# Performance work log

Measured on AMD Instinct MI355X. Metric: run time of the kernel, lower is better.

## Reference

```python
import jax, jax.numpy as jnp
import numpy as np

N = 100000
E = 1_600_000
IN_X, OUT_X = 128, 128
IN_E, OUT_E = 32, 128


def setup_inputs() -> dict:
    key = jax.random.key(0)
    k1, k2, k3, k4, k5, k6, k7 = jax.random.split(key, 7)
    x = jax.random.normal(k1, (N, IN_X), dtype=jnp.float32)
    edge_index = jax.random.randint(k2, (2, E), 0, N, dtype=jnp.int64)
    edge_attr = jax.random.normal(k3, (E, IN_E), dtype=jnp.float32)
    Wx = jax.random.normal(k4, (IN_X, OUT_X), dtype=jnp.float32) * (1.0 / np.sqrt(IN_X))
    bx = jax.random.normal(k5, (OUT_X,), dtype=jnp.float32) * 0.01
    We = jax.random.normal(k6, (IN_E, OUT_E), dtype=jnp.float32) * (1.0 / np.sqrt(IN_E))
    be = jax.random.normal(k7, (OUT_E,), dtype=jnp.float32) * 0.01
    return {"x": x, "edge_index": edge_index, "edge_attr": edge_attr,
            "Wx": Wx, "bx": bx, "We": We, "be": be}


def reference(x, edge_index, edge_attr, Wx, bx, We, be):
    # torch: to_dense() -> [N, N, in_e]; sum over dim=1 == scatter-add of
    # edge_attr into rows indexed by the source node edge_index[0].
    agg = jax.ops.segment_sum(edge_attr, edge_index[0], num_segments=x.shape[0])  # [N, in_e]
    hx = x @ Wx + bx          # [N, out_x]
    he = agg @ We + be        # [N, out_e]
    return jnp.concatenate((hx, he), axis=1)  # [N, out_x + out_e]
```

## Files before the change

kernel.cpp:

```cpp
#include <hip/hip_runtime.h>


#define BSHIFT    7
#define BSIZE     128
#define NBMAX     1024
#define SEG_CAP   3584
#define POOL_SZ   3648
#define CHUNK_A   8192
#define SPILL_CAP 65536

typedef short bf16x8 __attribute__((ext_vector_type(8)));
typedef float f32x4  __attribute__((ext_vector_type(4)));

__device__ __forceinline__ unsigned short f2bf(float f) {
    union { float f; unsigned u; } c; c.f = f;
    unsigned u = c.u;
    u += 0x7FFF + ((u >> 16) & 1);
    return (unsigned short)(u >> 16);
}

__global__ __launch_bounds__(512) void binA_kernel(
    const int* __restrict__ src, int E, int nb,
    unsigned* __restrict__ segs, int* __restrict__ gcnt,
    int2* __restrict__ spill, int* __restrict__ spillcnt)
{
    __shared__ unsigned pool[CHUNK_A];
    __shared__ int hist[NBMAX];
    __shared__ int offs[NBMAX];
    __shared__ int lcur[NBMAX];
    __shared__ int gbase[NBMAX];
    __shared__ int gallow[NBMAX];
    __shared__ int wsum[8];

    int tid = threadIdx.x;
    int base = blockIdx.x * CHUNK_A;

    for (int i = tid; i < NBMAX; i += 512) hist[i] = 0;
    __syncthreads();

    for (int i = tid; i < CHUNK_A; i += 512) {
        int e = base + i;
        if (e < E) atomicAdd(&hist[src[e] >> BSHIFT], 1);
    }
    __syncthreads();

    {
        int t2 = tid * 2;
        int c0 = hist[t2], c1 = hist[t2 + 1];
        int s = c0 + c1;
        int lane = tid & 63, wid = tid >> 6;
        int ws = s;
        #pragma unroll
        for (int d = 1; d < 64; d <<= 1) {
            int t = __shfl_up(ws, d);
            if (lane >= d) ws += t;
        }
        if (lane == 63) wsum[wid] = ws;
        __syncthreads();
        int woff = 0;
        #pragma unroll
        for (int w = 0; w < 8; ++w) if (w < wid) woff += wsum[w];
        int ex = woff + ws - s;
        offs[t2] = ex;          lcur[t2] = ex;
        offs[t2 + 1] = ex + c0; lcur[t2 + 1] = ex + c0;
    }
    __syncthreads();

    {
        int t2 = tid * 2;
        #pragma unroll
        for (int u = 0; u < 2; ++u) {
            int b = t2 + u;
            if (b < nb) {
                int cnt = hist[b];
                int b0 = cnt ? atomicAdd(&gcnt[b], cnt) : 0;
                gbase[b] = b0;
                int allow = SEG_CAP - b0;
                if (allow < 0) allow = 0;
                if (allow > cnt) allow = cnt;
                gallow[b] = allow;
            }
        }
    }
    __syncthreads();

    for (int i = tid; i < CHUNK_A; i += 512) {
        int e = base + i;
        if (e < E) {
            int s = src[e];
            int b = s >> BSHIFT;
            int p = atomicAdd(&lcur[b], 1);
            pool[p] = ((unsigned)e << BSHIFT) | (unsigned)(s & (BSIZE - 1));
        }
    }
    __syncthreads();

    int wid = tid >> 6, lane = tid & 63;
    for (int b = wid; b < nb; b += 8) {
        int cnt = hist[b];
        int off = offs[b];
        int allow = gallow[b];
        unsigned* dst = segs + (size_t)b * SEG_CAP + gbase[b];
        for (int i = lane; i < allow; i += 64)
            dst[i] = pool[off + i];
        int excess = cnt - allow;
        if (excess > 0) {
            int sb;
            if (lane == 0) sb = atomicAdd(spillcnt, excess);
            sb = __shfl(sb, 0);
            for (int i = lane; i < excess; i += 64) {
                int sp = sb + i;
                if (sp < SPILL_CAP) {
                    unsigned pv = pool[off + allow + i];
                    spill[sp] = make_int2((int)(pv >> BSHIFT),
                                          (b << BSHIFT) | (int)(pv & (BSIZE - 1)));
                }
            }
        }
    }
}

__global__ __launch_bounds__(512) void gather_kernel(
    const unsigned* __restrict__ segs, const int* __restrict__ gcnt,
    const int2* __restrict__ spill, const int* __restrict__ spillcnt,
    const float4* __restrict__ ea4, unsigned short* __restrict__ aggbf, int N)
{
    __shared__ int counts[BSIZE];
    __shared__ int starts[BSIZE + 1];
    __shared__ int cursor[BSIZE];
    __shared__ int pool[POOL_SZ];

    int tid = threadIdx.x;
    int b = blockIdx.x;
    int node0 = b << BSHIFT;

    if (tid < BSIZE) counts[tid] = 0;
    __syncthreads();

    int segn = gcnt[b]; if (segn > SEG_CAP) segn = SEG_CAP;
    const unsigned* seg = segs + (size_t)b * SEG_CAP;
    int nsp = *spillcnt; if (nsp > SPILL_CAP) nsp = SPILL_CAP;

    for (int i = tid; i < segn; i += 512)
        atomicAdd(&counts[seg[i] & (BSIZE - 1)], 1);
    if (nsp)
        for (int i = tid; i < nsp; i += 512) {
            int2 p = spill[i];
            if ((p.y >> BSHIFT) == b) atomicAdd(&counts[p.y & (BSIZE - 1)], 1);
        }
    __syncthreads();

    if (tid < 64) {
        int c0 = counts[tid * 2], c1 = counts[tid * 2 + 1];
        int s = c0 + c1;
        int ws = s;
        #pragma unroll
        for (int d = 1; d < 64; d <<= 1) {
            int t = __shfl_up(ws, d);
            if (tid >= d) ws += t;
        }
        int ex = ws - s;
        starts[tid * 2] = ex;          cursor[tid * 2] = ex;
        starts[tid * 2 + 1] = ex + c0; cursor[tid * 2 + 1] = ex + c0;
        if (tid == 63) starts[BSIZE] = ws;
    }
    __syncthreads();

    for (int i = tid; i < segn; i += 512) {
        unsigned pe = seg[i];
        int pos = atomicAdd(&cursor[pe & (BSIZE - 1)], 1);
        if (pos < POOL_SZ) pool[pos] = (int)(pe >> BSHIFT);
    }
    if (nsp)
        for (int i = tid; i < nsp; i += 512) {
            int2 p = spill[i];
            if ((p.y >> BSHIFT) == b) {
                int pos = atomicAdd(&cursor[p.y & (BSIZE - 1)], 1);
                if (pos < POOL_SZ) pool[pos] = p.x;
            }
        }
    __syncthreads();

    int g = tid >> 2, q2 = tid & 3;
    int node = node0 + g;
    if (node < N) {
        int p0 = starts[g], p1 = starts[g + 1];
        if (p1 > POOL_SZ) p1 = POOL_SZ;
        float4 aL0 = {0.f,0.f,0.f,0.f}, aL1 = {0.f,0.f,0.f,0.f};
        float4 aH0 = {0.f,0.f,0.f,0.f}, aH1 = {0.f,0.f,0.f,0.f};
        int p = p0;
        for (; p + 4 <= p1; p += 4) {
            int e0 = pool[p], e1 = pool[p + 1], e2 = pool[p + 2], e3 = pool[p + 3];
            const float4* r0 = ea4 + (size_t)e0 * 8;
            const float4* r1 = ea4 + (size_t)e1 * 8;
            const float4* r2 = ea4 + (size_t)e2 * 8;
            const float4* r3 = ea4 + (size_t)e3 * 8;
            float4 l0 = r0[q2],     l1 = r1[q2],     l2 = r2[q2],     l3 = r3[q2];
            float4 h0 = r0[q2 + 4], h1 = r1[q2 + 4], h2 = r2[q2 + 4], h3 = r3[q2 + 4];
            aL0.x += l0.x; aL0.y += l0.y; aL0.z += l0.z; aL0.w += l0.w;
            aL1.x += l1.x; aL1.y += l1.y; aL1.z += l1.z; aL1.w += l1.w;
            aH0.x += h0.x; aH0.y += h0.y; aH0.z += h0.z; aH0.w += h0.w;
            aH1.x += h1.x; aH1.y += h1.y; aH1.z += h1.z; aH1.w += h1.w;
            aL0.x += l2.x; aL0.y += l2.y; aL0.z += l2.z; aL0.w += l2.w;
            aL1.x += l3.x; aL1.y += l3.y; aL1.z += l3.z; aL1.w += l3.w;
            aH0.x += h2.x; aH0.y += h2.y; aH0.z += h2.z; aH0.w += h2.w;
            aH1.x += h3.x; aH1.y += h3.y; aH1.z += h3.z; aH1.w += h3.w;
        }
        for (; p < p1; ++p) {
            const float4* r = ea4 + (size_t)pool[p] * 8;
            float4 l = r[q2], h = r[q2 + 4];
            aL0.x += l.x; aL0.y += l.y; aL0.z += l.z; aL0.w += l.w;
            aH0.x += h.x; aH0.y += h.y; aH0.z += h.z; aH0.w += h.w;
        }
        aL0.x += aL1.x; aL0.y += aL1.y; aL0.z += aL1.z; aL0.w += aL1.w;
        aH0.x += aH1.x; aH0.y += aH1.y; aH0.z += aH1.z; aH0.w += aH1.w;
        uint2 lo, hi;
        lo.x = (unsigned)f2bf(aL0.x) | ((unsigned)f2bf(aL0.y) << 16);
        lo.y = (unsigned)f2bf(aL0.z) | ((unsigned)f2bf(aL0.w) << 16);
        hi.x = (unsigned)f2bf(aH0.x) | ((unsigned)f2bf(aH0.y) << 16);
        hi.y = (unsigned)f2bf(aH0.z) | ((unsigned)f2bf(aH0.w) << 16);
        *(uint2*)(aggbf + (size_t)node * 32 + q2 * 4)       = lo;
        *(uint2*)(aggbf + (size_t)node * 32 + (q2 + 4) * 4) = hi;
    }
}

__global__ __launch_bounds__(256) void scatter_kernel(
    const float4* __restrict__ ea4, const int* __restrict__ src,
    float* __restrict__ agg, int nquads)
{
    int t = blockIdx.x * blockDim.x + threadIdx.x;
    if (t >= nquads) return;
    int e = t >> 3, q = t & 7;
    float4 v = ea4[t];
    int node = src[e];
    float* dst = agg + (size_t)node * 32 + q * 4;
    atomicAdd(dst + 0, v.x); atomicAdd(dst + 1, v.y);
    atomicAdd(dst + 2, v.z); atomicAdd(dst + 3, v.w);
}

__global__ __launch_bounds__(256) void cvt_kernel(
    const float* __restrict__ agg, unsigned short* __restrict__ aggbf, int n)
{
    int t = blockIdx.x * blockDim.x + threadIdx.x;
    if (t < n) aggbf[t] = f2bf(agg[t]);
}

__global__ __launch_bounds__(512, 4) void mfma_gemm(
    const float* __restrict__ x, const unsigned short* __restrict__ aggbf,
    const float* __restrict__ Wx, const float* __restrict__ bx,
    const float* __restrict__ We, const float* __restrict__ be,
    float* __restrict__ out, int N, int ntiles)
{
    __shared__ char sWxT[128 * 256];
    __shared__ char sWeT[128 * 64];
    __shared__ char sX[128 * 256];
    __shared__ char sA[128 * 64];

    int tid = threadIdx.x;
    int lane = tid & 63, w = tid >> 6;
    int col = lane & 15, m = lane >> 4;

    for (int i = tid; i < 128 * 128; i += 512) {
        int k = i >> 7, j = i & 127;
        *(unsigned short*)(sWxT + j * 256 + ((k * 2) ^ ((j & 7) << 4))) = f2bf(Wx[i]);
    }
    for (int i = tid; i < 32 * 128; i += 512) {
        int k = i >> 7, j = i & 127;
        *(unsigned short*)(sWeT + j * 64 + ((k * 2) ^ ((j & 3) << 4))) = f2bf(We[i]);
    }
    float bxv[8], bev[8];
    #pragma unroll
    for (int ct = 0; ct < 8; ++ct) {
        bxv[ct] = bx[ct * 16 + col];
        bev[ct] = be[ct * 16 + col];
    }

    int lrow = (w << 4) + col;
    int swzA = (lrow & 7) << 4;

    for (int t = blockIdx.x; t < ntiles; t += gridDim.x) {
        int rbase_t = t << 7;
        __syncthreads();

        for (int i = tid; i < 128 * 32; i += 512) {
            int row = i >> 5, c4 = i & 31;
            int gr = rbase_t + row;
            float4 v = {0.f, 0.f, 0.f, 0.f};
            if (gr < N) v = *(const float4*)(x + (size_t)gr * 128 + c4 * 4);
            uint2 uu;
            uu.x = (unsigned)f2bf(v.x) | ((unsigned)f2bf(v.y) << 16);
            uu.y = (unsigned)f2bf(v.z) | ((unsigned)f2bf(v.w) << 16);
            *(uint2*)(sX + ((row * 256 + c4 * 8) ^ ((row & 7) << 4))) = uu;
        }
        {
            int row = tid >> 2, mm = tid & 3;
            int gr = rbase_t + row;
            bf16x8 av = {0, 0, 0, 0, 0, 0, 0, 0};
            if (gr < N) av = *(const bf16x8*)(aggbf + (size_t)gr * 32 + mm * 8);
            *(bf16x8*)(sA + ((row * 64 + mm * 16) ^ ((row & 7) << 4))) = av;
        }
        __syncthreads();

        bf16x8 ax[4];
        #pragma unroll
        for (int kk = 0; kk < 4; ++kk)
            ax[kk] = *(const bf16x8*)(sX + lrow * 256 + ((kk * 64 + m * 16) ^ swzA));
        bf16x8 aa = *(const bf16x8*)(sA + ((lrow * 64 + m * 16) ^ swzA));

        int srow = rbase_t + (w << 4) + m * 4;

        #pragma unroll
        for (int half = 0; half < 2; ++half) {
            f32x4 acc[8];
            #pragma unroll
            for (int ct = 0; ct < 4; ++ct) {
                int c8 = half * 4 + ct;
                acc[ct]     = (f32x4){bxv[c8], bxv[c8], bxv[c8], bxv[c8]};
                acc[4 + ct] = (f32x4){bev[c8], bev[c8], bev[c8], bev[c8]};
            }

            #pragma unroll
            for (int ct = 0; ct < 4; ++ct) {
                int c8 = half * 4 + ct;
                const char* brow = sWxT + (c8 * 16 + col) * 256;
                int swz = (col & 7) << 4;
                #pragma unroll
                for (int kk = 0; kk < 4; ++kk) {
                    bf16x8 bfrag = *(const bf16x8*)(brow + ((kk * 64 + m * 16) ^ swz));
                    acc[ct] = __builtin_amdgcn_mfma_f32_16x16x32_bf16(ax[kk], bfrag, acc[ct], 0, 0, 0);
                }
                bf16x8 bwe = *(const bf16x8*)(sWeT + (c8 * 16 + col) * 64 + ((m * 16) ^ ((col & 3) << 4)));
                acc[4 + ct] = __builtin_amdgcn_mfma_f32_16x16x32_bf16(aa, bwe, acc[4 + ct], 0, 0, 0);
            }

            #pragma unroll
            for (int r = 0; r < 4; ++r) {
                if (srow + r < N) {
                    float* orow = out + (size_t)(srow + r) * 256 + col + half * 64;
                    #pragma unroll
                    for (int ct = 0; ct < 4; ++ct) {
                        orow[ct * 16]       = acc[ct][r];
                        orow[128 + ct * 16] = acc[4 + ct][r];
                    }
                }
            }
        }
    }
}

extern "C" void kernel_launch(void* const* d_in, const int* in_sizes, int n_in,
                              void* d_out, int out_size, void* d_ws, size_t ws_size,
                              hipStream_t stream) {
    const float* x          = (const float*)d_in[0];
    const int*   edge_index = (const int*)d_in[1];
    const float* edge_attr  = (const float*)d_in[2];
    const float* Wx         = (const float*)d_in[3];
    const float* bx         = (const float*)d_in[4];
    const float* We         = (const float*)d_in[5];
    const float* be         = (const float*)d_in[6];
    float* out = (float*)d_out;

    int N = in_sizes[0] / 128;
    int E = in_sizes[2] / 32;
    int nb = (N + BSIZE - 1) >> BSHIFT;
    int ntiles = (N + 127) >> 7;

    char* ws = (char*)d_ws;
    size_t aggbfBytes = ((size_t)N * 32 * 2 + 255) & ~255ull;
    size_t segsBytes  = ((size_t)nb * SEG_CAP * 4 + 255) & ~255ull;
    size_t gcntBytes  = ((size_t)(nb + 1) * 4 + 255) & ~255ull;
    size_t spillBytes = (size_t)SPILL_CAP * 8;
    size_t need = aggbfBytes + segsBytes + gcntBytes + spillBytes;

    unsigned short* aggbf = (unsigned short*)ws;

    if (ws_size >= need && nb <= NBMAX) {
        unsigned* segs  = (unsigned*)(ws + aggbfBytes);
        int* gcnt       = (int*)(ws + aggbfBytes + segsBytes);
        int* spillcnt   = gcnt + nb;
        int2* spill     = (int2*)(ws + aggbfBytes + segsBytes + gcntBytes);

        hipMemsetAsync(gcnt, 0, (size_t)(nb + 1) * 4, stream);
        int nblkA = (E + CHUNK_A - 1) / CHUNK_A;
        binA_kernel<<<nblkA, 512, 0, stream>>>(edge_index, E, nb, segs, gcnt, spill, spillcnt);
        gather_kernel<<<nb, 512, 0, stream>>>(segs, gcnt, spill, spillcnt,
                                              (const float4*)edge_attr, aggbf, N);
    } else {
        float* aggf = (float*)(ws + aggbfBytes);
        hipMemsetAsync(aggf, 0, (size_t)N * 32 * 4, stream);
        int nq = E * 8;
        scatter_kernel<<<(nq + 255) / 256, 256, 0, stream>>>(
            (const float4*)edge_attr, edge_index, aggf, nq);
        cvt_kernel<<<(N * 32 + 255) / 256, 256, 0, stream>>>(aggf, aggbf, N * 32);
    }

    int g = ntiles < 512 ? ntiles : 512;
    mfma_gemm<<<g, 512, 0, stream>>>(x, aggbf, Wx, bx, We, be, out, N, ntiles);
}
```

Before: 171.0 us.

## Fuse edge-feature GEMM into gather kernel, drop bf16 aggregate round trip

```diff
diff --git a/kernel.cpp b/kernel.cpp
--- a/kernel.cpp
+++ b/kernel.cpp
@@ -120,21 +120,31 @@
     }
 }
 
-__global__ __launch_bounds__(512) void gather_kernel(
+__global__ __launch_bounds__(512) void gather_he_kernel(
     const unsigned* __restrict__ segs, const int* __restrict__ gcnt,
     const int2* __restrict__ spill, const int* __restrict__ spillcnt,
-    const float4* __restrict__ ea4, unsigned short* __restrict__ aggbf, int N)
+    const float4* __restrict__ ea4,
+    const float* __restrict__ We, const float* __restrict__ be,
+    float* __restrict__ out, int N)
 {
     __shared__ int counts[BSIZE];
     __shared__ int starts[BSIZE + 1];
     __shared__ int cursor[BSIZE];
     __shared__ int pool[POOL_SZ];
+    __shared__ char sAgg[BSIZE * 64];
+    __shared__ char sWeT[128 * 64];
 
     int tid = threadIdx.x;
     int b = blockIdx.x;
     int node0 = b << BSHIFT;
+    int lane = tid & 63, w = tid >> 6;
+    int col = lane & 15, m = lane >> 4;
 
     if (tid < BSIZE) counts[tid] = 0;
+    for (int i = tid; i < 32 * 128; i += 512) {
+        int k = i >> 7, j = i & 127;
+        *(unsigned short*)(sWeT + j * 64 + ((k * 2) ^ ((j & 3) << 4))) = f2bf(We[i]);
+    }
     __syncthreads();
 
     int segn = gcnt[b]; if (segn > SEG_CAP) segn = SEG_CAP;
@@ -181,46 +191,78 @@
         }
     __syncthreads();
 
-    int g = tid >> 2, q2 = tid & 3;
-    int node = node0 + g;
-    if (node < N) {
-        int p0 = starts[g], p1 = starts[g + 1];
-        if (p1 > POOL_SZ) p1 = POOL_SZ;
+    {
+        int g = tid >> 2, q2 = tid & 3;
+        int node = node0 + g;
         float4 aL0 = {0.f,0.f,0.f,0.f}, aL1 = {0.f,0.f,0.f,0.f};
         float4 aH0 = {0.f,0.f,0.f,0.f}, aH1 = {0.f,0.f,0.f,0.f};
-        int p = p0;
-        for (; p + 4 <= p1; p += 4) {
-            int e0 = pool[p], e1 = pool[p + 1], e2 = pool[p + 2], e3 = pool[p + 3];
-            const float4* r0 = ea4 + (size_t)e0 * 8;
-            const float4* r1 = ea4 + (size_t)e1 * 8;
-            const float4* r2 = ea4 + (size_t)e2 * 8;
-            const float4* r3 = ea4 + (size_t)e3 * 8;
-            float4 l0 = r0[q2],     l1 = r1[q2],     l2 = r2[q2],     l3 = r3[q2];
-            float4 h0 = r0[q2 + 4], h1 = r1[q2 + 4], h2 = r2[q2 + 4], h3 = r3[q2 + 4];
-            aL0.x += l0.x; aL0.y += l0.y; aL0.z += l0.z; aL0.w += l0.w;
-            aL1.x += l1.x; aL1.y += l1.y; aL1.z += l1.z; aL1.w += l1.w;
-            aH0.x += h0.x; aH0.y += h0.y; aH0.z += h0.z; aH0.w += h0.w;
-            aH1.x += h1.x; aH1.y += h1.y; aH1.z += h1.z; aH1.w += h1.w;
-            aL0.x += l2.x; aL0.y += l2.y; aL0.z += l2.z; aL0.w += l2.w;
-            aL1.x += l3.x; aL1.y += l3.y; aL1.z += l3.z; aL1.w += l3.w;
-            aH0.x += h2.x; aH0.y += h2.y; aH0.z += h2.z; aH0.w += h2.w;
-            aH1.x += h3.x; aH1.y += h3.y; aH1.z += h3.z; aH1.w += h3.w;
-        }
-        for (; p < p1; ++p) {
-            const float4* r = ea4 + (size_t)pool[p] * 8;
-            float4 l = r[q2], h = r[q2 + 4];
-            aL0.x += l.x; aL0.y += l.y; aL0.z += l.z; aL0.w += l.w;
-            aH0.x += h.x; aH0.y += h.y; aH0.z += h.z; aH0.w += h.w;
-        }
-        aL0.x += aL1.x; aL0.y += aL1.y; aL0.z += aL1.z; aL0.w += aL1.w;
-        aH0.x += aH1.x; aH0.y += aH1.y; aH0.z += aH1.z; aH0.w += aH1.w;
+        if (node < N) {
+            int p0 = starts[g], p1 = starts[g + 1];
+            if (p1 > POOL_SZ) p1 = POOL_SZ;
+            int p = p0;
+            for (; p + 4 <= p1; p += 4) {
+                int e0 = pool[p], e1 = pool[p + 1], e2 = pool[p + 2], e3 = pool[p + 3];
+                const float4* r0 = ea4 + (size_t)e0 * 8;
+                const float4* r1 = ea4 + (size_t)e1 * 8;
+                const float4* r2 = ea4 + (size_t)e2 * 8;
+                const float4* r3 = ea4 + (size_t)e3 * 8;
+                float4 l0 = r0[q2],     l1 = r1[q2],     l2 = r2[q2],     l3 = r3[q2];
+                float4 h0 = r0[q2 + 4], h1 = r1[q2 + 4], h2 = r2[q2 + 4], h3 = r3[q2 + 4];
+                aL0.x += l0.x; aL0.y += l0.y; aL0.z += l0.z; aL0.w += l0.w;
+                aL1.x += l1.x; aL1.y += l1.y; aL1.z += l1.z; aL1.w += l1.w;
+                aH0.x += h0.x; aH0.y += h0.y; aH0.z += h0.z; aH0.w += h0.w;
+                aH1.x += h1.x; aH1.y += h1.y; aH1.z += h1.z; aH1.w += h1.w;
+                aL0.x += l2.x; aL0.y += l2.y; aL0.z += l2.z; aL0.w += l2.w;
+                aL1.x += l3.x; aL1.y += l3.y; aL1.z += l3.z; aL1.w += l3.w;
+                aH0.x += h2.x; aH0.y += h2.y; aH0.z += h2.z; aH0.w += h2.w;
+                aH1.x += h3.x; aH1.y += h3.y; aH1.z += h3.z; aH1.w += h3.w;
+            }
+            for (; p < p1; ++p) {
+                const float4* r = ea4 + (size_t)pool[p] * 8;
+                float4 l = r[q2], h = r[q2 + 4];
+                aL0.x += l.x; aL0.y += l.y; aL0.z += l.z; aL0.w += l.w;
+                aH0.x += h.x; aH0.y += h.y; aH0.z += h.z; aH0.w += h.w;
+            }
+            aL0.x += aL1.x; aL0.y += aL1.y; aL0.z += aL1.z; aL0.w += aL1.w;
+            aH0.x += aH1.x; aH0.y += aH1.y; aH0.z += aH1.z; aH0.w += aH1.w;
+        }
         uint2 lo, hi;
         lo.x = (unsigned)f2bf(aL0.x) | ((unsigned)f2bf(aL0.y) << 16);
         lo.y = (unsigned)f2bf(aL0.z) | ((unsigned)f2bf(aL0.w) << 16);
         hi.x = (unsigned)f2bf(aH0.x) | ((unsigned)f2bf(aH0.y) << 16);
         hi.y = (unsigned)f2bf(aH0.z) | ((unsigned)f2bf(aH0.w) << 16);
-        *(uint2*)(aggbf + (size_t)node * 32 + q2 * 4)       = lo;
-        *(uint2*)(aggbf + (size_t)node * 32 + (q2 + 4) * 4) = hi;
+        int swz = (g & 7) << 4;
+        *(uint2*)(sAgg + ((g * 64 + q2 * 8) ^ swz))            = lo;
+        *(uint2*)(sAgg + ((g * 64 + (q2 + 4) * 8) ^ swz))      = hi;
+    }
+    __syncthreads();
+
+    {
+        int lrow = (w << 4) + col;
+        bf16x8 aa = *(const bf16x8*)(sAgg + ((lrow * 64 + m * 16) ^ ((lrow & 7) << 4)));
+
+        f32x4 acc[8];
+        #pragma unroll
+        for (int ct = 0; ct < 8; ++ct) {
+            float bv = be[ct * 16 + col];
+            acc[ct] = (f32x4){bv, bv, bv, bv};
+        }
+        #pragma unroll
+        for (int ct = 0; ct < 8; ++ct) {
+            bf16x8 bwe = *(const bf16x8*)(sWeT + (ct * 16 + col) * 64 + ((m * 16) ^ ((col & 3) << 4)));
+            acc[ct] = __builtin_amdgcn_mfma_f32_16x16x32_bf16(aa, bwe, acc[ct], 0, 0, 0);
+        }
+
+        int srow = node0 + (w << 4) + m * 4;
+        #pragma unroll
+        for (int r = 0; r < 4; ++r) {
+            if (srow + r < N) {
+                float* orow = out + (size_t)(srow + r) * 256 + 128 + col;
+                #pragma unroll
+                for (int ct = 0; ct < 8; ++ct)
+                    orow[ct * 16] = acc[ct][r];
+            }
+        }
     }
 }
 
@@ -245,6 +287,7 @@
     if (t < n) aggbf[t] = f2bf(agg[t]);
 }
 
+template <bool DO_HE>
 __global__ __launch_bounds__(512, 4) void mfma_gemm(
     const float* __restrict__ x, const unsigned short* __restrict__ aggbf,
     const float* __restrict__ Wx, const float* __restrict__ bx,
@@ -264,15 +307,16 @@
         int k = i >> 7, j = i & 127;
         *(unsigned short*)(sWxT + j * 256 + ((k * 2) ^ ((j & 7) << 4))) = f2bf(Wx[i]);
     }
-    for (int i = tid; i < 32 * 128; i += 512) {
-        int k = i >> 7, j = i & 127;
-        *(unsigned short*)(sWeT + j * 64 + ((k * 2) ^ ((j & 3) << 4))) = f2bf(We[i]);
-    }
+    if (DO_HE)
+        for (int i = tid; i < 32 * 128; i += 512) {
+            int k = i >> 7, j = i & 127;
+            *(unsigned short*)(sWeT + j * 64 + ((k * 2) ^ ((j & 3) << 4))) = f2bf(We[i]);
+        }
     float bxv[8], bev[8];
     #pragma unroll
     for (int ct = 0; ct < 8; ++ct) {
         bxv[ct] = bx[ct * 16 + col];
-        bev[ct] = be[ct * 16 + col];
+        if (DO_HE) bev[ct] = be[ct * 16 + col];
     }
 
     int lrow = (w << 4) + col;
@@ -292,7 +336,7 @@
             uu.y = (unsigned)f2bf(v.z) | ((unsigned)f2bf(v.w) << 16);
             *(uint2*)(sX + ((row * 256 + c4 * 8) ^ ((row & 7) << 4))) = uu;
         }
-        {
+        if (DO_HE) {
             int row = tid >> 2, mm = tid & 3;
             int gr = rbase_t + row;
             bf16x8 av = {0, 0, 0, 0, 0, 0, 0, 0};
@@ -305,7 +349,8 @@
         #pragma unroll
         for (int kk = 0; kk < 4; ++kk)
             ax[kk] = *(const bf16x8*)(sX + lrow * 256 + ((kk * 64 + m * 16) ^ swzA));
-        bf16x8 aa = *(const bf16x8*)(sA + ((lrow * 64 + m * 16) ^ swzA));
+        bf16x8 aa = {0,0,0,0,0,0,0,0};
+        if (DO_HE) aa = *(const bf16x8*)(sA + ((lrow * 64 + m * 16) ^ swzA));
 
         int srow = rbase_t + (w << 4) + m * 4;
 
@@ -315,8 +360,8 @@
             #pragma unroll
             for (int ct = 0; ct < 4; ++ct) {
                 int c8 = half * 4 + ct;
-                acc[ct]     = (f32x4){bxv[c8], bxv[c8], bxv[c8], bxv[c8]};
-                acc[4 + ct] = (f32x4){bev[c8], bev[c8], bev[c8], bev[c8]};
+                acc[ct] = (f32x4){bxv[c8], bxv[c8], bxv[c8], bxv[c8]};
+                if (DO_HE) acc[4 + ct] = (f32x4){bev[c8], bev[c8], bev[c8], bev[c8]};
             }
 
             #pragma unroll
@@ -329,8 +374,10 @@
                     bf16x8 bfrag = *(const bf16x8*)(brow + ((kk * 64 + m * 16) ^ swz));
                     acc[ct] = __builtin_amdgcn_mfma_f32_16x16x32_bf16(ax[kk], bfrag, acc[ct], 0, 0, 0);
                 }
-                bf16x8 bwe = *(const bf16x8*)(sWeT + (c8 * 16 + col) * 64 + ((m * 16) ^ ((col & 3) << 4)));
-                acc[4 + ct] = __builtin_amdgcn_mfma_f32_16x16x32_bf16(aa, bwe, acc[4 + ct], 0, 0, 0);
+                if (DO_HE) {
+                    bf16x8 bwe = *(const bf16x8*)(sWeT + (c8 * 16 + col) * 64 + ((m * 16) ^ ((col & 3) << 4)));
+                    acc[4 + ct] = __builtin_amdgcn_mfma_f32_16x16x32_bf16(aa, bwe, acc[4 + ct], 0, 0, 0);
+                }
             }
 
             #pragma unroll
@@ -339,8 +386,8 @@
                     float* orow = out + (size_t)(srow + r) * 256 + col + half * 64;
                     #pragma unroll
                     for (int ct = 0; ct < 4; ++ct) {
-                        orow[ct * 16]       = acc[ct][r];
-                        orow[128 + ct * 16] = acc[4 + ct][r];
+                        orow[ct * 16] = acc[ct][r];
+                        if (DO_HE) orow[128 + ct * 16] = acc[4 + ct][r];
                     }
                 }
             }
@@ -374,6 +421,8 @@
 
     unsigned short* aggbf = (unsigned short*)ws;
 
+    int g = ntiles < 512 ? ntiles : 512;
+
     if (ws_size >= need && nb <= NBMAX) {
         unsigned* segs  = (unsigned*)(ws + aggbfBytes);
         int* gcnt       = (int*)(ws + aggbfBytes + segsBytes);
@@ -383,8 +432,9 @@
         hipMemsetAsync(gcnt, 0, (size_t)(nb + 1) * 4, stream);
         int nblkA = (E + CHUNK_A - 1) / CHUNK_A;
         binA_kernel<<<nblkA, 512, 0, stream>>>(edge_index, E, nb, segs, gcnt, spill, spillcnt);
-        gather_kernel<<<nb, 512, 0, stream>>>(segs, gcnt, spill, spillcnt,
-                                              (const float4*)edge_attr, aggbf, N);
+        gather_he_kernel<<<nb, 512, 0, stream>>>(segs, gcnt, spill, spillcnt,
+                                                 (const float4*)edge_attr, We, be, out, N);
+        mfma_gemm<false><<<g, 512, 0, stream>>>(x, aggbf, Wx, bx, We, be, out, N, ntiles);
     } else {
         float* aggf = (float*)(ws + aggbfBytes);
         hipMemsetAsync(aggf, 0, (size_t)N * 32 * 4, stream);
@@ -392,8 +442,6 @@
         scatter_kernel<<<(nq + 255) / 256, 256, 0, stream>>>(
             (const float4*)edge_attr, edge_index, aggf, nq);
         cvt_kernel<<<(N * 32 + 255) / 256, 256, 0, stream>>>(aggf, aggbf, N * 32);
-    }
-
-    int g = ntiles < 512 ? ntiles : 512;
-    mfma_gemm<<<g, 512, 0, stream>>>(x, aggbf, Wx, bx, We, be, out, N, ntiles);
-}
+        mfma_gemm<true><<<g, 512, 0, stream>>>(x, aggbf, Wx, bx, We, be, out, N, ntiles);
+    }
+}
```

After: 150.4 us. 12.0% less time.
